# Optimization experiments

Hardware: AMD Instinct MI355X
Metric: run time of the kernel (lower is better)

Reference implementation:

```python
import jax, jax.numpy as jnp
import numpy as np
from jax import lax

BLANK_ID = 0
NEG_INF = -1e10  # finite stand-in for log(0); module uses LOG_0 = -1e10

B, T, H, V, L = 32, 1000, 512, 2048, 100


def setup_inputs() -> dict:
    key = jax.random.key(0)
    k1, k2, k3, k4, k5, k6 = jax.random.split(key, 6)
    eouts = jax.random.normal(k1, (B, T, H), dtype=jnp.float32)
    W = jax.random.normal(k2, (V, H), dtype=jnp.float32) * (1.0 / np.sqrt(H))
    b = jax.random.normal(k3, (V,), dtype=jnp.float32) * 0.01
    ys = jax.random.randint(k4, (B, L), 1, V, dtype=jnp.int32)  # labels exclude blank=0
    ylens = jax.random.randint(k5, (B,), L // 2, L + 1, dtype=jnp.int32)
    # ensure T_b >= 2*L_b + 1 so every alignment is feasible
    elens = jnp.clip(jax.random.randint(k6, (B,), T // 2, T + 1, dtype=jnp.int32), 2 * L + 1, T)
    return {"eouts": eouts, "W": W, "b": b, "ys": ys, "elens": elens, "ylens": ylens}


def ctc_loss_sum(log_probs, ys, elens, ylens):
    """Batched CTC forward DP. log_probs: [B,T,V]; ys: [B,L]; returns sum loss."""
    Bb, Tt, Vv = log_probs.shape
    Ll = ys.shape[1]
    S = 2 * Ll + 1
    # extended label sequence: blank, y1, blank, y2, ..., blank
    ext = jnp.zeros((Bb, S), dtype=jnp.int32).at[:, 1::2].set(ys)
    # gather per-frame log-probs of extended labels: [B,T,S]
    lp_ext = jnp.take_along_axis(log_probs, jnp.broadcast_to(ext[:, None, :], (Bb, Tt, S)), axis=2)
    # s-2 skip allowed iff ext[s] != blank and ext[s] != ext[s-2]
    ext_m2 = jnp.pad(ext, ((0, 0), (2, 0)), constant_values=-1)[:, :S]
    skip_ok = (ext != BLANK_ID) & (ext != ext_m2)
    valid = jnp.arange(S)[None, :] < (2 * ylens[:, None] + 1)  # [B,S]

    a0 = jnp.full((Bb, S), NEG_INF, dtype=log_probs.dtype)
    a0 = a0.at[:, 0].set(lp_ext[:, 0, 0]).at[:, 1].set(lp_ext[:, 0, 1])
    a0 = jnp.where(valid, a0, NEG_INF)

    def step(a, lp_t):  # a: [B,S], lp_t: [B,S]
        a1 = a
        a2 = jnp.pad(a, ((0, 0), (1, 0)), constant_values=NEG_INF)[:, :S]
        a3 = jnp.where(skip_ok, jnp.pad(a, ((0, 0), (2, 0)), constant_values=NEG_INF)[:, :S], NEG_INF)
        new = jnp.logaddexp(jnp.logaddexp(a1, a2), a3) + lp_t
        new = jnp.where(valid, new, NEG_INF)
        return new, new

    _, alphas_rest = lax.scan(step, a0, jnp.swapaxes(lp_ext, 0, 1)[1:])  # [T-1,B,S]
    alphas = jnp.concatenate([a0[None], alphas_rest], axis=0)  # [T,B,S]

    a_final = alphas[elens - 1, jnp.arange(Bb)]  # [B,S]
    last = jnp.take_along_axis(a_final, (2 * ylens)[:, None], axis=1)[:, 0]
    prev = jnp.take_along_axis(a_final, (2 * ylens - 1)[:, None], axis=1)[:, 0]
    loss_b = -jnp.logaddexp(last, prev)
    # zero_infinity=True: replace non-finite (numerically huge) losses with 0
    loss_b = jnp.where(loss_b < -0.5 * NEG_INF, loss_b, 0.0)
    return jnp.sum(loss_b)


def reference(eouts, W, b, ys, elens, ylens):
    logits = jnp.einsum("bth,vh->btv", eouts, W) + b  # self.output(eouts)
    log_probs = jax.nn.log_softmax(logits, axis=-1)
    loss_ctc = ctc_loss_sum(log_probs, ys, elens, ylens) / eouts.shape[0]
    return loss_ctc
```

## Files before the change

### kernel.cpp

```cpp
#include <hip/hip_runtime.h>
#include <hip/hip_bf16.h>

#define B_ 32
#define T_ 1000
#define H_ 512
#define V_ 2048
#define L_ 100
#define M_ (B_*T_)
#define GSTRIDE 104
#define LOG2E 1.4426950408889634f
#define LSE_SHIFT 48.0f
#define BIAS60 1.152921504606847e18f

typedef __attribute__((ext_vector_type(8))) short bf16x8;
typedef __attribute__((ext_vector_type(4))) float f32x4;

#define AS_G(p)  ((const __attribute__((address_space(1))) unsigned int*)(p))
#define AS_L(p)  ((__attribute__((address_space(3))) unsigned int*)(p))

__device__ __forceinline__ unsigned short f2bf(float x) {
    unsigned int u; __builtin_memcpy(&u, &x, 4);
    unsigned int r = (u + 0x7fffu + ((u >> 16) & 1u)) >> 16;
    return (unsigned short)r;
}

__device__ __forceinline__ float dpp_shr1(float x) {
    int r = __builtin_amdgcn_update_dpp(0, __builtin_bit_cast(int, x), 0x138, 0xf, 0xf, false);
    return __builtin_bit_cast(float, r);
}
template<int CTRL>
__device__ __forceinline__ float fmax_dpp(float x) {
    int s = __builtin_amdgcn_update_dpp(0, __builtin_bit_cast(int, x), CTRL, 0xf, 0xf, false);
    return fmaxf(x, __builtin_bit_cast(float, s));
}
__device__ __forceinline__ float wave_max_nonneg(float x) {
    x = fmax_dpp<0x111>(x);
    x = fmax_dpp<0x112>(x);
    x = fmax_dpp<0x114>(x);
    x = fmax_dpp<0x118>(x);
    x = fmax_dpp<0x142>(x);
    x = fmax_dpp<0x143>(x);
    return __builtin_bit_cast(float, __builtin_amdgcn_readlane(__builtin_bit_cast(int, x), 63));
}

__global__ __launch_bounds__(256) void prep_kernel(
        const float* __restrict__ eouts, const float* __restrict__ W,
        unsigned short* __restrict__ eb, unsigned short* __restrict__ wb,
        float* __restrict__ Srow, float* __restrict__ out)
{
    const int E4 = M_*H_/4;
    const int W4 = V_*H_/4;
    const int S4 = M_/4;
    int idx = blockIdx.x*256 + threadIdx.x;
    if (idx == 0) out[0] = 0.f;
    if (idx < E4) {
        float4 v = ((const float4*)eouts)[idx];
        ushort4 o; o.x=f2bf(v.x); o.y=f2bf(v.y); o.z=f2bf(v.z); o.w=f2bf(v.w);
        ((ushort4*)eb)[idx] = o;
    } else if (idx < E4 + W4) {
        int j = idx - E4;
        float4 v = ((const float4*)W)[j];
        ushort4 o; o.x=f2bf(v.x); o.y=f2bf(v.y); o.z=f2bf(v.z); o.w=f2bf(v.w);
        ((ushort4*)wb)[j] = o;
    } else if (idx < E4 + W4 + S4) {
        int j = idx - E4 - W4;
        ((float4*)Srow)[j] = make_float4(0.f,0.f,0.f,0.f);
    }
}

__global__ __launch_bounds__(512, 1) void gemm_lse_kernel(
        const unsigned short* __restrict__ eb, const unsigned short* __restrict__ wb,
        const float* __restrict__ bias, float* __restrict__ Srow)
{
    __shared__ __align__(16) unsigned short Ab[2][256*64];
    __shared__ __align__(16) unsigned short Bb[2][256*64];
    __shared__ float rs[256];
    const int tid  = threadIdx.x;
    const int w    = tid >> 6;
    const int lane = tid & 63;
    const int m    = lane & 15;
    const int qh   = lane >> 4;
    const int wr   = w >> 2;
    const int wc   = w & 3;
    const int rl   = m & 7;
    const int lrow = lane >> 3;
    const int k8   = ((lane & 7) ^ lrow) * 8;
    const int nbase = blockIdx.x * 256;
    const int ytile = blockIdx.y;
    const int ntiles = (124 - ytile)/32 + 1;
    int mb_cur = ytile * 256;

    if (tid < 256) rs[tid] = 0.f;

    f32x4 acc[8][4];
    #pragma unroll
    for (int i=0;i<8;i++)
        #pragma unroll
        for (int j=0;j<4;j++) acc[i][j] = (f32x4){0.f,0.f,0.f,0.f};
    bf16x8 af[2][2], bfr[4][2];

#define STAGE_A(sel, r, kt, mb) do { \
        const unsigned short* _s = eb + (size_t)((mb) + (r)*64 + w*8 + lrow)*H_ + (kt)*64 + k8; \
        __builtin_amdgcn_global_load_lds(AS_G(_s), AS_L(&Ab[sel][((r)*64 + w*8)*64]), 16, 0, 0); \
    } while(0)
#define STAGE_B(sel, r, kt) do { \
        const unsigned short* _s = wb + (size_t)(nbase + (r)*64 + w*8 + lrow)*H_ + (kt)*64 + k8; \
        __builtin_amdgcn_global_load_lds(AS_G(_s), AS_L(&Bb[sel][((r)*64 + w*8)*64]), 16, 0, 0); \
    } while(0)

#define LOADB(sel) \
    _Pragma("unroll") \
    for (int ni=0; ni<4; ++ni) { \
        const int brow = wc*64 + ni*16 + m; \
        bfr[ni][0] = *(const bf16x8*)(&Bb[sel][brow*64 + ((qh ^ rl))*8]); \
        bfr[ni][1] = *(const bf16x8*)(&Bb[sel][brow*64 + (((4+qh) ^ rl))*8]); \
    }
#define LOADA(sel, qq) \
    _Pragma("unroll") \
    for (int mi2=0; mi2<2; ++mi2) { \
        const int arow = wr*128 + ((qq)*2+mi2)*16 + m; \
        af[mi2][0] = *(const bf16x8*)(&Ab[sel][arow*64 + ((qh ^ rl))*8]); \
        af[mi2][1] = *(const bf16x8*)(&Ab[sel][arow*64 + (((4+qh) ^ rl))*8]); \
    }
#define MFMA16(qq) \
    __builtin_amdgcn_s_setprio(1); \
    _Pragma("unroll") \
    for (int mi2=0; mi2<2; ++mi2) \
        _Pragma("unroll") \
        for (int ni=0; ni<4; ++ni) { \
            acc[(qq)*2+mi2][ni] = __builtin_amdgcn_mfma_f32_16x16x32_bf16(af[mi2][0], bfr[ni][0], acc[(qq)*2+mi2][ni], 0, 0, 0); \
            acc[(qq)*2+mi2][ni] = __builtin_amdgcn_mfma_f32_16x16x32_bf16(af[mi2][1], bfr[ni][1], acc[(qq)*2+mi2][ni], 0, 0, 0); \
        } \
    __builtin_amdgcn_s_setprio(0);
#define BARX() __builtin_amdgcn_s_barrier()
#define WAIT_LGKM() do { asm volatile("s_waitcnt lgkmcnt(0)" ::: "memory"); \
                         __builtin_amdgcn_sched_barrier(0); } while(0)

    STAGE_B(0,0,0); STAGE_B(0,1,0);
    STAGE_B(0,2,0); STAGE_B(0,3,0);
    STAGE_A(0,1,0,mb_cur); STAGE_A(0,3,0,mb_cur);
    STAGE_A(0,0,0,mb_cur); STAGE_A(0,2,0,mb_cur);
    STAGE_B(1,0,1); STAGE_B(1,1,1);
    STAGE_B(1,2,1); STAGE_B(1,3,1);
    STAGE_A(1,1,1,mb_cur); STAGE_A(1,3,1,mb_cur);
    asm volatile("s_waitcnt vmcnt(6)" ::: "memory");
    BARX();

    #pragma unroll 1
    for (int mt = 0; mt < ntiles; ++mt) {
        const int mb_nxt = (ytile + 32*(mt+1)) * 256;
        #pragma unroll 1
        for (int it = 0; it < 4; ++it) {
            const bool last = (mt == ntiles-1) && (it == 3);
            const int k1 = 2*it + 1;
            const int k2 = (2*it + 2) & 7;
            const int k3 = (2*it + 3) & 7;
            const int mbs = (it < 3) ? mb_cur : mb_nxt;
            LOADB(0) LOADA(0,3)
            STAGE_A(1,0,k1,mb_cur); STAGE_A(1,2,k1,mb_cur);
            BARX(); WAIT_LGKM();
            MFMA16(3)
            BARX();
            LOADA(0,2)
            if (!last) { STAGE_B(0,0,k2); STAGE_B(0,1,k2); }
            BARX(); WAIT_LGKM();
            MFMA16(2)
            BARX();
            LOADA(0,1)
            if (!last) { STAGE_B(0,2,k2); STAGE_B(0,3,k2); }
            BARX(); WAIT_LGKM();
            MFMA16(1)
            BARX();
            LOADA(0,0)
            if (!last) { STAGE_A(0,1,k2,mbs); STAGE_A(0,3,k2,mbs); }
            BARX(); WAIT_LGKM();
            MFMA16(0)
            if (!last) { asm volatile("s_waitcnt vmcnt(6)" ::: "memory"); }
            else       { asm volatile("s_waitcnt vmcnt(0)" ::: "memory"); }
            BARX();
            LOADB(1) LOADA(1,3)
            if (!last) { STAGE_A(0,0,k2,mbs); STAGE_A(0,2,k2,mbs); }
            BARX(); WAIT_LGKM();
            MFMA16(3)
            BARX();
            LOADA(1,2)
            if (!last) { STAGE_B(1,0,k3); STAGE_B(1,1,k3); }
            BARX(); WAIT_LGKM();
            MFMA16(2)
            BARX();
            LOADA(1,1)
            if (!last) { STAGE_B(1,2,k3); STAGE_B(1,3,k3); }
            BARX(); WAIT_LGKM();
            MFMA16(1)
            BARX();
            LOADA(1,0)
            if (!last) { STAGE_A(1,1,k3,mbs); STAGE_A(1,3,k3,mbs); }
            BARX(); WAIT_LGKM();
            MFMA16(0)
            if (!last) { asm volatile("s_waitcnt vmcnt(6)" ::: "memory"); }
            else       { asm volatile("s_waitcnt vmcnt(0)" ::: "memory"); }
            BARX();
        }

        {
            float bv[4];
            #pragma unroll
            for (int ni=0;ni<4;ni++) bv[ni] = bias[nbase + wc*64 + ni*16 + m];
            #pragma unroll
            for (int mi=0;mi<8;mi++) {
                #pragma unroll
                for (int r=0;r<4;r++) {
                    float s = 0.f;
                    #pragma unroll
                    for (int ni=0;ni<4;ni++)
                        s += exp2f((acc[mi][ni][r] + bv[ni]) * LOG2E - LSE_SHIFT);
                    s += __shfl_xor(s, 1);
                    s += __shfl_xor(s, 2);
                    s += __shfl_xor(s, 4);
                    s += __shfl_xor(s, 8);
                    if (m == 0) atomicAdd(&rs[wr*128 + mi*16 + qh*4 + r], s);
                }
            }
            WAIT_LGKM();
            BARX();
            if (tid < 256) {
                atomicAdd(&Srow[mb_cur + tid], rs[tid]);
                rs[tid] = 0.f;
            }
            #pragma unroll
            for (int i=0;i<8;i++)
                #pragma unroll
                for (int j=0;j<4;j++) acc[i][j] = (f32x4){0.f,0.f,0.f,0.f};
        }
        mb_cur = mb_nxt;
    }
#undef STAGE_A
#undef STAGE_B
#undef LOADB
#undef LOADA
#undef MFMA16
#undef BARX
#undef WAIT_LGKM
}

__global__ __launch_bounds__(256) void gather_mfma_kernel(
        const unsigned short* __restrict__ eb, const unsigned short* __restrict__ wb,
        const float* __restrict__ bias, const int* __restrict__ ys,
        const float* __restrict__ Srow, float* __restrict__ g)
{
    __shared__ __align__(16) unsigned short As[128*64];
    __shared__ __align__(16) unsigned short Bs[128*64];
    __shared__ float ls[128];
    const int tid  = threadIdx.x;
    const int w    = tid >> 6;
    const int lane = tid & 63;
    const int m    = lane & 15;
    const int q    = lane >> 4;
    const int wrow = w >> 1;
    const int wcol = w & 1;
    const int b    = blockIdx.y;
    const int tb   = blockIdx.x * 128;

    if (tid < 128) {
        int t = tb + tid;
        ls[tid] = (t < T_) ? (LSE_SHIFT + log2f(Srow[b*T_ + t])) : 0.f;
    }

    const int rbase = w*32 + (lane >> 3);
    const int k8    = (((lane & 7) ^ ((lane >> 3) & 7)) * 8);
    const int rl    = m & 7;

    int vrow[4];
    #pragma unroll
    for (int j=0;j<4;++j) {
        int labr = rbase + j*8;
        vrow[j] = (labr == 0 || labr > L_) ? 0 : ys[b*L_ + labr - 1];
    }
    int labc[4]; float bv[4];
    #pragma unroll
    for (int ni=0;ni<4;++ni) {
        int lab = wcol*64 + ni*16 + m;
        labc[ni] = lab;
        int v = (lab == 0 || lab > L_) ? 0 : ys[b*L_ + lab - 1];
        bv[ni] = bias[v];
    }

    f32x4 acc[4][4];
    #pragma unroll
    for (int i=0;i<4;i++)
        #pragma unroll
        for (int j=0;j<4;j++) acc[i][j] = (f32x4){0.f,0.f,0.f,0.f};

    for (int kc = 0; kc < 8; ++kc) {
        __syncthreads();
        #pragma unroll
        for (int j = 0; j < 4; ++j) {
            const unsigned short* ga = eb + (size_t)(b*T_ + tb + rbase + j*8)*H_ + kc*64 + k8;
            __builtin_amdgcn_global_load_lds(AS_G(ga), AS_L(As + (w*4+j)*512), 16, 0, 0);
            const unsigned short* gw = wb + (size_t)vrow[j]*H_ + kc*64 + k8;
            __builtin_amdgcn_global_load_lds(AS_G(gw), AS_L(Bs + (w*4+j)*512), 16, 0, 0);
        }
        __syncthreads();
        #pragma unroll
        for (int kk = 0; kk < 2; ++kk) {
            const int sw = ((kk*4 + q) ^ rl) * 8;
            bf16x8 af[4], bfr[4];
            #pragma unroll
            for (int mi=0;mi<4;mi++)
                af[mi] = *(const bf16x8*)(As + (wrow*8 + mi*2 + (m>>3))*512 + rl*64 + sw);
            #pragma unroll
            for (int ni=0;ni<4;ni++)
                bfr[ni] = *(const bf16x8*)(Bs + (wcol*8 + ni*2 + (m>>3))*512 + rl*64 + sw);
            #pragma unroll
            for (int mi=0;mi<4;mi++)
                #pragma unroll
                for (int ni=0;ni<4;ni++)
                    acc[mi][ni] = __builtin_amdgcn_mfma_f32_16x16x32_bf16(
                        af[mi], bfr[ni], acc[mi][ni], 0, 0, 0);
        }
    }

    #pragma unroll
    for (int mi=0;mi<4;mi++) {
        #pragma unroll
        for (int r=0;r<4;r++) {
            int trow = wrow*64 + mi*16 + q*4 + r;
            int t = tb + trow;
            float l2 = ls[trow];
            #pragma unroll
            for (int ni=0;ni<4;ni++) {
                if (t < T_ && labc[ni] <= L_) {
                    float p = exp2f((acc[mi][ni][r] + bv[ni]) * LOG2E - l2);
                    int off = (labc[ni] == 0) ? 0 : labc[ni] + 1;
                    g[(size_t)(b*T_ + t)*GSTRIDE + off] = p;
                }
            }
        }
    }
}

__global__ __launch_bounds__(128, 1) void ctc_dp_kernel(
        const float* __restrict__ g, const int* __restrict__ ys,
        const int* __restrict__ elens, const int* __restrict__ ylens,
        float* __restrict__ out)
{
    __shared__ __align__(16) float ring[2*2048];
    const int b    = blockIdx.x;
    const int tid  = threadIdx.x;
    const int wv   = tid >> 6;
    const int lane = tid & 63;
    const float* gb = g + (size_t)b * T_ * GSTRIDE;
    const int ylen = ylens[b];
    const int elen = elens[b];
    const int kmax = (elen - 1) >> 4;

    const int Sv   = 2*ylen + 1;
    const int s0   = 4*lane;
    const float msk0 = (s0   < Sv) ? 1.f : 0.f;
    const float msk1 = (s0+1 < Sv) ? 1.f : 0.f;
    const float msk2 = (s0+2 < Sv) ? 1.f : 0.f;
    const float msk3 = (s0+3 < Sv) ? 1.f : 0.f;
    const int l0 = 2*lane, l1 = 2*lane + 1;
    int i0 = min(max(l0,1), L_-1);
    int i1 = min(l1, L_-1);
    const float sk1 = (l0 >= 1 && l0 < L_ && ys[b*L_+i0] != ys[b*L_+i0-1]) ? 1.f : 0.f;
    const float sk3 = (l1 < L_        && ys[b*L_+i1] != ys[b*L_+i1-1]) ? 1.f : 0.f;

    float a0 = 0.f, a1 = 0.f, a2 = 0.f, a3 = 0.f, C2 = 0.f;
    if (wv == 0) {
        a0 = (lane == 0) ? gb[0] : 0.f;
        a1 = (lane == 0) ? gb[2] : 0.f;
    } else {
        #pragma unroll
        for (int s = 0; s < 8; ++s) {
            int srow = min(2*s, T_-2);
            __builtin_amdgcn_global_load_lds(AS_G(gb + (size_t)srow*GSTRIDE + 4*lane),
                                             AS_L(ring + s*256), 16, 0, 0);
        }
    }

    auto dpstep = [&](float p0, float p1, float p2, float p3) {
        float um1 = dpp_shr1(a3);
        float n0 = a0 + um1;
        float n1 = a1 + a0 + sk1*um1;
        float n2 = a2 + a1;
        float n3 = a3 + a2 + sk3*a1;
        a0 = n0*p0; a1 = n1*p1; a2 = n2*p2; a3 = n3*p3;
    };
    auto renorm = [&]() {
        float mm = wave_max_nonneg(fmaxf(fmaxf(a0,a1), fmaxf(a2,a3)));
        if (mm > 0.f) {
            float rr = fminf(__fdividef(BIAS60, mm), 3.0e38f);
            C2 -= __log2f(rr);
            a0 *= rr; a1 *= rr; a2 *= rr; a3 *= rr;
        }
    };

    __syncthreads();

    for (int k = 0; k <= kmax; ++k) {
        if (wv == 1) {
            if (k < kmax) {
                float* dset = ring + ((k+1) & 1)*2048;
                int pbase = 8*(k + 1);
                #pragma unroll
                for (int s = 0; s < 8; ++s) {
                    int srow = min(2*(pbase + s), T_-2);
                    __builtin_amdgcn_global_load_lds(AS_G(gb + (size_t)srow*GSTRIDE + 4*lane),
                                                     AS_L(dset + s*256), 16, 0, 0);
                }
            }
        } else {
            const float* sb = ring + (k & 1)*2048;
            float P0[16], P1[16], P2[16], P3[16];
            #pragma unroll
            for (int s = 0; s < 8; ++s) {
                const float* slot = sb + s*256;
                float pb0 = slot[0];
                float pb1 = slot[104];
                float2 lo = *(const float2*)(slot + 2  + 2*lane);
                float2 hi = *(const float2*)(slot + 106 + 2*lane);
                P0[2*s]   = pb0*msk0; P1[2*s]   = lo.x*msk1;
                P2[2*s]   = pb0*msk2; P3[2*s]   = lo.y*msk3;
                P0[2*s+1] = pb1*msk0; P1[2*s+1] = hi.x*msk1;
                P2[2*s+1] = pb1*msk2; P3[2*s+1] = hi.y*msk3;
            }
            const int t0 = 16*k;
            #pragma unroll
            for (int j = 0; j < 16; ++j) {
                int t = t0 + j;
                if (t > 0 && t < elen)
                    dpstep(P0[j], P1[j], P2[j], P3[j]);
                if ((j & 7) == 7) renorm();
            }
        }
        __syncthreads();
    }

    if (wv == 0) {
        int sA = 2*ylen, sB = sA - 1;
        float vA = __shfl((sA & 2) ? a2 : a0, sA >> 2);
        float vB = __shfl((sB & 2) ? a3 : a1, sB >> 2);
        if (lane == 0) {
            float sum = vA + vB;
            float loss = 0.f;
            if (sum > 0.f) {
                loss = -(log2f(sum) + C2) * 0.6931471805599453f;
                if (!(loss < 5e9f)) loss = 0.f;
            }
            atomicAdd(out, loss * (1.0f/B_));
        }
    }
}

extern "C" void kernel_launch(void* const* d_in, const int* in_sizes, int n_in,
                              void* d_out, int out_size, void* d_ws, size_t ws_size,
                              hipStream_t stream)
{
    const float* eouts = (const float*)d_in[0];
    const float* W     = (const float*)d_in[1];
    const float* bias  = (const float*)d_in[2];
    const int*   ys    = (const int*)d_in[3];
    const int*   elens = (const int*)d_in[4];
    const int*   ylens = (const int*)d_in[5];
    float* out = (float*)d_out;

    char* ws = (char*)d_ws;
    unsigned short* eb = (unsigned short*)ws;
    unsigned short* wb = (unsigned short*)(ws + 32768000);
    float* Srow        = (float*)(ws + 34865152);
    float* g           = (float*)(ws + 34993152);

    prep_kernel<<<17057, 256, 0, stream>>>(eouts, W, eb, wb, Srow, out);
    gemm_lse_kernel<<<dim3(8, 32), 512, 0, stream>>>(eb, wb, bias, Srow);
    gather_mfma_kernel<<<dim3(8, 32), 256, 0, stream>>>(eb, wb, bias, ys, Srow, g);
    ctc_dp_kernel<<<B_, 128, 0, stream>>>(g, ys, elens, ylens, out);
}
```

Measured before the change: 276.8 us.

## Drop LDS waitcnts, use DPP row sums with direct global atomics in GEMM-LSE

Removes the explicit lgkmcnt(0) waits and scheduling barriers after each LDS fragment load and leaves wait placement to the compiler. The LDS row-sum staging buffer is replaced by a DPP row reduction plus direct global atomicAdd into Srow. Bias loads are hoisted out of the tile loop, MFMA issue order is regrouped by k-half, and the grid is linearised so consecutive blocks share an N column. Without the explicit waits, correctness depends on the compiler inserting the right lgkmcnt, and direct global atomics raise the atomic traffic to Srow.

```diff
diff --git a/kernel.cpp b/kernel.cpp
--- a/kernel.cpp
+++ b/kernel.cpp
@@ -41,6 +41,18 @@
     x = fmax_dpp<0x142>(x);
     x = fmax_dpp<0x143>(x);
     return __builtin_bit_cast(float, __builtin_amdgcn_readlane(__builtin_bit_cast(int, x), 63));
+}
+template<int CTRL>
+__device__ __forceinline__ float fadd_dpp(float x) {
+    int s = __builtin_amdgcn_update_dpp(0, __builtin_bit_cast(int, x), CTRL, 0xf, 0xf, false);
+    return x + __builtin_bit_cast(float, s);
+}
+__device__ __forceinline__ float rowsum16(float x) {
+    x = fadd_dpp<0x111>(x);
+    x = fadd_dpp<0x112>(x);
+    x = fadd_dpp<0x114>(x);
+    x = fadd_dpp<0x118>(x);
+    return x;
 }
 
 __global__ __launch_bounds__(256) void prep_kernel(
@@ -74,7 +86,6 @@
 {
     __shared__ __align__(16) unsigned short Ab[2][256*64];
     __shared__ __align__(16) unsigned short Bb[2][256*64];
-    __shared__ float rs[256];
     const int tid  = threadIdx.x;
     const int w    = tid >> 6;
     const int lane = tid & 63;
@@ -85,12 +96,15 @@
     const int rl   = m & 7;
     const int lrow = lane >> 3;
     const int k8   = ((lane & 7) ^ lrow) * 8;
-    const int nbase = blockIdx.x * 256;
-    const int ytile = blockIdx.y;
+    const int lin   = blockIdx.x;
+    const int ytile = lin & 31;
+    const int nbase = (lin >> 5) * 256;
     const int ntiles = (124 - ytile)/32 + 1;
     int mb_cur = ytile * 256;
 
-    if (tid < 256) rs[tid] = 0.f;
+    float bv[4];
+    #pragma unroll
+    for (int ni=0;ni<4;ni++) bv[ni] = bias[nbase + wc*64 + ni*16 + m];
 
     f32x4 acc[8][4];
     #pragma unroll
@@ -127,14 +141,15 @@
     _Pragma("unroll") \
     for (int mi2=0; mi2<2; ++mi2) \
         _Pragma("unroll") \
-        for (int ni=0; ni<4; ++ni) { \
+        for (int ni=0; ni<4; ++ni) \
             acc[(qq)*2+mi2][ni] = __builtin_amdgcn_mfma_f32_16x16x32_bf16(af[mi2][0], bfr[ni][0], acc[(qq)*2+mi2][ni], 0, 0, 0); \
+    _Pragma("unroll") \
+    for (int mi2=0; mi2<2; ++mi2) \
+        _Pragma("unroll") \
+        for (int ni=0; ni<4; ++ni) \
             acc[(qq)*2+mi2][ni] = __builtin_amdgcn_mfma_f32_16x16x32_bf16(af[mi2][1], bfr[ni][1], acc[(qq)*2+mi2][ni], 0, 0, 0); \
-        } \
     __builtin_amdgcn_s_setprio(0);
 #define BARX() __builtin_amdgcn_s_barrier()
-#define WAIT_LGKM() do { asm volatile("s_waitcnt lgkmcnt(0)" ::: "memory"); \
-                         __builtin_amdgcn_sched_barrier(0); } while(0)
 
     STAGE_B(0,0,0); STAGE_B(0,1,0);
     STAGE_B(0,2,0); STAGE_B(0,3,0);
@@ -158,80 +173,67 @@
             const int mbs = (it < 3) ? mb_cur : mb_nxt;
             LOADB(0) LOADA(0,3)
             STAGE_A(1,0,k1,mb_cur); STAGE_A(1,2,k1,mb_cur);
-            BARX(); WAIT_LGKM();
+            BARX();
             MFMA16(3)
             BARX();
             LOADA(0,2)
             if (!last) { STAGE_B(0,0,k2); STAGE_B(0,1,k2); }
-            BARX(); WAIT_LGKM();
+            BARX();
             MFMA16(2)
             BARX();
             LOADA(0,1)
             if (!last) { STAGE_B(0,2,k2); STAGE_B(0,3,k2); }
-            BARX(); WAIT_LGKM();
+            BARX();
             MFMA16(1)
             BARX();
             LOADA(0,0)
             if (!last) { STAGE_A(0,1,k2,mbs); STAGE_A(0,3,k2,mbs); }
-            BARX(); WAIT_LGKM();
+            BARX();
             MFMA16(0)
             if (!last) { asm volatile("s_waitcnt vmcnt(6)" ::: "memory"); }
             else       { asm volatile("s_waitcnt vmcnt(0)" ::: "memory"); }
             BARX();
             LOADB(1) LOADA(1,3)
             if (!last) { STAGE_A(0,0,k2,mbs); STAGE_A(0,2,k2,mbs); }
-            BARX(); WAIT_LGKM();
+            BARX();
             MFMA16(3)
             BARX();
             LOADA(1,2)
             if (!last) { STAGE_B(1,0,k3); STAGE_B(1,1,k3); }
-            BARX(); WAIT_LGKM();
+            BARX();
             MFMA16(2)
             BARX();
             LOADA(1,1)
             if (!last) { STAGE_B(1,2,k3); STAGE_B(1,3,k3); }
-            BARX(); WAIT_LGKM();
+            BARX();
             MFMA16(1)
             BARX();
             LOADA(1,0)
             if (!last) { STAGE_A(1,1,k3,mbs); STAGE_A(1,3,k3,mbs); }
-            BARX(); WAIT_LGKM();
+            BARX();
             MFMA16(0)
             if (!last) { asm volatile("s_waitcnt vmcnt(6)" ::: "memory"); }
             else       { asm volatile("s_waitcnt vmcnt(0)" ::: "memory"); }
             BARX();
         }
 
-        {
-            float bv[4];
-            #pragma unroll
-            for (int ni=0;ni<4;ni++) bv[ni] = bias[nbase + wc*64 + ni*16 + m];
-            #pragma unroll
-            for (int mi=0;mi<8;mi++) {
+        #pragma unroll
+        for (int mi=0;mi<8;mi++) {
+            #pragma unroll
+            for (int r=0;r<4;r++) {
+                float s = 0.f;
                 #pragma unroll
-                for (int r=0;r<4;r++) {
-                    float s = 0.f;
-                    #pragma unroll
-                    for (int ni=0;ni<4;ni++)
-                        s += exp2f((acc[mi][ni][r] + bv[ni]) * LOG2E - LSE_SHIFT);
-                    s += __shfl_xor(s, 1);
-                    s += __shfl_xor(s, 2);
-                    s += __shfl_xor(s, 4);
-                    s += __shfl_xor(s, 8);
-                    if (m == 0) atomicAdd(&rs[wr*128 + mi*16 + qh*4 + r], s);
-                }
-            }
-            WAIT_LGKM();
-            BARX();
-            if (tid < 256) {
-                atomicAdd(&Srow[mb_cur + tid], rs[tid]);
-                rs[tid] = 0.f;
-            }
-            #pragma unroll
-            for (int i=0;i<8;i++)
-                #pragma unroll
-                for (int j=0;j<4;j++) acc[i][j] = (f32x4){0.f,0.f,0.f,0.f};
-        }
+                for (int ni=0;ni<4;ni++)
+                    s += exp2f((acc[mi][ni][r] + bv[ni]) * LOG2E - LSE_SHIFT);
+                s = rowsum16(s);
+                if (m == 15)
+                    atomicAdd(&Srow[mb_cur + wr*128 + mi*16 + qh*4 + r], s);
+            }
+        }
+        #pragma unroll
+        for (int i=0;i<8;i++)
+            #pragma unroll
+            for (int j=0;j<4;j++) acc[i][j] = (f32x4){0.f,0.f,0.f,0.f};
         mb_cur = mb_nxt;
     }
 #undef STAGE_A
@@ -240,7 +242,6 @@
 #undef LOADA
 #undef MFMA16
 #undef BARX
-#undef WAIT_LGKM
 }
 
 __global__ __launch_bounds__(256) void gather_mfma_kernel(
@@ -472,7 +473,7 @@
     float* g           = (float*)(ws + 34993152);
 
     prep_kernel<<<17057, 256, 0, stream>>>(eouts, W, eb, wb, Srow, out);
-    gemm_lse_kernel<<<dim3(8, 32), 512, 0, stream>>>(eb, wb, bias, Srow);
+    gemm_lse_kernel<<<256, 512, 0, stream>>>(eb, wb, bias, Srow);
     gather_mfma_kernel<<<dim3(8, 32), 256, 0, stream>>>(eb, wb, bias, ys, Srow, g);
     ctc_dp_kernel<<<B_, 128, 0, stream>>>(g, ys, elens, ylens, out);
 }
```

Result: no change. 271.9 us (-1.8%).
